# Kernel optimization log

Hardware: AMD Instinct MI355X
Metric: run time of the kernel (lower is better)

## Reference

```python
import jax, jax.numpy as jnp
from jax import lax
import numpy as np

D_MODEL = 1024
D_STATE = 16
D_CONV = 4
EXPAND = 2
D_INNER = EXPAND * D_MODEL  # 2048
BATCH = 4
SEQLEN = 2048


def setup_inputs() -> dict:
    key = jax.random.key(0)
    ks = jax.random.split(key, 8)
    s = 0.02  # small init scale for stability
    f32 = jnp.float32
    return {
        "x": jax.random.normal(ks[0], (BATCH, SEQLEN, D_MODEL), f32),
        # Linear weights stored as (in, out); torch applies x @ W.T with W (out, in) -- same math.
        "W_in": (jax.random.normal(ks[1], (D_MODEL, 2 * D_INNER), f32) * s),
        "conv_w": (jax.random.normal(ks[2], (D_INNER, 1, D_CONV), f32) * s),  # depthwise (O, I/groups=1, K)
        "conv_b": jnp.zeros((D_INNER,), f32),
        "W_xproj": (jax.random.normal(ks[3], (D_INNER, 2 * D_STATE), f32) * s),
        "W_dt": (jax.random.normal(ks[4], (D_INNER, D_INNER), f32) * s),
        "b_dt": jnp.zeros((D_INNER,), f32),
        "A_log": jnp.log(jax.random.uniform(ks[5], (D_INNER, D_STATE), f32, 1e-4, 1.0)),
        "D_param": jnp.ones((D_INNER,), f32),
        "W_out": (jax.random.normal(ks[6], (D_INNER, D_MODEL), f32) * s),
    }


def _mamba_forward(x, W_in, conv_w, conv_b, W_xproj, W_dt, b_dt, A_log, D_param, W_out):
    Bb, L, _ = x.shape
    # in_proj and split into x-branch and gate z
    xz = x @ W_in                      # (B, L, 2*d_inner)
    xc, z = jnp.split(xz, 2, axis=-1)
    # causal depthwise conv1d: torch pads both sides by d_conv-1 then slices [:L] == left-pad only
    xt = xc.transpose(0, 2, 1)         # (B, d_inner, L)
    xconv = lax.conv_general_dilated(
        xt, conv_w, window_strides=(1,), padding=[(D_CONV - 1, 0)],
        feature_group_count=D_INNER, dimension_numbers=("NCH", "OIH", "NCH"))
    xs = jax.nn.silu(xconv.transpose(0, 2, 1) + conv_b[None, None, :])  # (B, L, d_inner)
    # SSM inputs
    delta = jax.nn.softplus(xs @ W_dt + b_dt)          # (B, L, d_inner)
    Bs, Cs = jnp.split(xs @ W_xproj, 2, axis=-1)       # each (B, L, d_state)
    A = -jnp.exp(A_log)                                 # (d_inner, d_state)

    def step(h, inp):
        dt, bv, cv, xv = inp                            # (B,d_inner),(B,d_state),(B,d_state),(B,d_inner)
        dA = 1.0 + A[None] * dt[..., None]              # Euler discretization (B, d_inner, d_state)
        dB = bv[:, None, :] * (xv * dt)[..., None]
        h = h * dA + dB
        y = jnp.einsum("bds,bs->bd", h, cv) + D_param * xv
        return h, y

    inputs = (delta.transpose(1, 0, 2), Bs.transpose(1, 0, 2),
              Cs.transpose(1, 0, 2), xs.transpose(1, 0, 2))
    h0 = jnp.zeros((Bb, D_INNER, D_STATE), x.dtype)
    _, ys = lax.scan(step, h0, inputs)                  # ys: (L, B, d_inner)
    y = ys.transpose(1, 0, 2) * jax.nn.silu(z)          # gated output
    return y @ W_out                                    # (B, L, d_model)


def reference(x, W_in, conv_w, conv_b, W_xproj, W_dt, b_dt, A_log, D_param, W_out):
    return _mamba_forward(x, W_in, conv_w, conv_b, W_xproj, W_dt, b_dt, A_log, D_param, W_out)
```

## Files before the change

### kernel.cpp

```cpp
#include <hip/hip_runtime.h>

#define AS1 __attribute__((address_space(1)))
#define AS3 __attribute__((address_space(3)))

typedef unsigned short u16;
typedef unsigned int u32;
typedef __attribute__((ext_vector_type(8))) __bf16 bf16x8;
typedef __attribute__((ext_vector_type(8))) unsigned short u16x8;
typedef __attribute__((ext_vector_type(4))) float f32x4;

#define BATCH   4
#define SEQLEN  2048
#define DMODEL  1024
#define DINNER  2048
#define DSTATE  16
#define ROWS    (BATCH * SEQLEN)

__device__ __forceinline__ u16 f2bf(float f) {
  union { float f; unsigned u; } v; v.f = f;
  unsigned u = v.u;
  return (u16)((u + 0x7fffu + ((u >> 16) & 1u)) >> 16);
}
__device__ __forceinline__ float bf2f(u16 s) {
  union { unsigned u; float f; } v; v.u = ((unsigned)s) << 16;
  return v.f;
}
__device__ __forceinline__ float bflo(u32 p) { union { unsigned u; float f; } v; v.u = p << 16; return v.f; }
__device__ __forceinline__ float bfhi(u32 p) { union { unsigned u; float f; } v; v.u = p & 0xffff0000u; return v.f; }

__global__ void cast_f32_bf16(const float* __restrict__ in, u16* __restrict__ out, int n4) {
  int i = blockIdx.x * blockDim.x + threadIdx.x;
  if (i >= n4) return;
  float4 v = ((const float4*)in)[i];
  ushort4 o;
  o.x = f2bf(v.x); o.y = f2bf(v.y); o.z = f2bf(v.z); o.w = f2bf(v.w);
  ((ushort4*)out)[i] = o;
}

__global__ void transpose_cast(const float* __restrict__ in, u16* __restrict__ out, int R, int C) {
  __shared__ float tile[32][33];
  int x  = blockIdx.x * 32 + threadIdx.x;
  int y0 = blockIdx.y * 32;
#pragma unroll
  for (int j = 0; j < 32; j += 8)
    tile[threadIdx.y + j][threadIdx.x] = in[(size_t)(y0 + threadIdx.y + j) * C + x];
  __syncthreads();
  int xo  = blockIdx.y * 32 + threadIdx.x;
  int yo0 = blockIdx.x * 32;
#pragma unroll
  for (int j = 0; j < 32; j += 8)
    out[(size_t)(yo0 + threadIdx.y + j) * R + xo] = f2bf(tile[threadIdx.x][threadIdx.y + j]);
}

template<int EPI, int BN_>
__launch_bounds__(512, 1)
__global__ void gemm8p(const u16* __restrict__ A, const u16* __restrict__ Bt,
                       void* __restrict__ outp, const float* __restrict__ bias,
                       int M, int N, int K, int gn, int rr, int cc) {
  constexpr int NF   = BN_ / 64;
  constexpr int BCH  = BN_ / 64;
  constexpr int ASZ  = 256 * 64;
  constexpr int BSZ  = BN_ * 64;
  constexpr int BUFS = ASZ + BSZ;
  extern __shared__ u16 lds[];

  const int xcd = blockIdx.x & 7, kb = blockIdx.x >> 3;
  const int tpr = gn / cc;
  const int bm  = (xcd / tpr) * rr + kb / cc;
  const int bn  = (xcd % tpr) * cc + kb % cc;

  const int tid  = threadIdx.x;
  const int wave = tid >> 6, lane = tid & 63;
  const int wm = wave >> 2, wn = wave & 3;
  const int llo = lane & 15, lhi = lane >> 4;
  const size_t bm0 = (size_t)bm * 256, bn0 = (size_t)bn * BN_;
  const int NT = K >> 6;

  const u16* gA[4];
#pragma unroll
  for (int ch = 0; ch < 4; ++ch) {
    int row  = ch * 64 + (tid >> 3);
    int scol = ((tid & 7) ^ (row & 7)) << 3;
    gA[ch] = A + (bm0 + row) * (size_t)K + scol;
  }
  const u16* gB[BCH];
#pragma unroll
  for (int ch = 0; ch < BCH; ++ch) {
    int row  = ch * 64 + (tid >> 3);
    int scol = ((tid & 7) ^ (row & 7)) << 3;
    gB[ch] = Bt + (bn0 + row) * (size_t)K + scol;
  }

  const int mask = (llo & 7) << 4;
  const int ko[2] = { ((0 + lhi * 16) ^ mask) >> 1, ((64 + lhi * 16) ^ mask) >> 1 };

#define SGA(t, bsel, ch) __builtin_amdgcn_global_load_lds(                       \
    (const AS1 void*)(gA[ch] + ((size_t)(t) << 6)),                              \
    (AS3 void*)(lds + (bsel) * BUFS + (ch) * 4096 + wave * 512), 16, 0, 0)
#define SGB(t, bsel, ch) __builtin_amdgcn_global_load_lds(                       \
    (const AS1 void*)(gB[ch] + ((size_t)(t) << 6)),                              \
    (AS3 void*)(lds + (bsel) * BUFS + ASZ + (ch) * 4096 + wave * 512), 16, 0, 0)

  f32x4 acc[8][NF] = {};
  bf16x8 bfr[2][NF];

#define PHASE(la_, lb_, MH, KK, RDB, STG, WC)                                    \
  {                                                                              \
    bf16x8 af[4];                                                                \
    _Pragma("unroll") for (int m = 0; m < 4; ++m)                                \
      af[m] = *(const bf16x8*)(const void*)((la_) + (wm*128 + MH*64 + m*16 + llo)*64 + ko[KK]); \
    if (RDB) {                                                                   \
      _Pragma("unroll") for (int n = 0; n < NF; ++n)                             \
        bfr[KK][n] = *(const bf16x8*)(const void*)((lb_) + (wn*(16*NF) + n*16 + llo)*64 + ko[KK]); \
    }                                                                            \
    STG;                                                                         \
    __builtin_amdgcn_s_barrier();                                                \
    __builtin_amdgcn_s_setprio(1);                                               \
    _Pragma("unroll") for (int m = 0; m < 4; ++m)                                \
      _Pragma("unroll") for (int n = 0; n < NF; ++n)                             \
        acc[MH*4+m][n] = __builtin_amdgcn_mfma_f32_16x16x32_bf16(af[m], bfr[KK][n], acc[MH*4+m][n], 0, 0, 0); \
    __builtin_amdgcn_s_setprio(0);                                               \
    WC;                                                                          \
    __builtin_amdgcn_s_barrier();                                                \
  }

  SGA(0, 0, 0); SGA(0, 0, 2); SGB(0, 0, 0); SGB(0, 0, 1);
  if (BCH == 4) { SGB(0, 0, 2); SGB(0, 0, 3); }
  SGA(0, 0, 1); SGA(0, 0, 3);
  SGA(1, 1, 0); SGA(1, 1, 2); SGB(1, 1, 0); SGB(1, 1, 1);
  asm volatile("s_waitcnt vmcnt(4)" ::: "memory");
  __builtin_amdgcn_s_barrier();

  const u16* la0 = lds;            const u16* lb0 = lds + ASZ;
  const u16* la1 = lds + BUFS;     const u16* lb1 = la1 + ASZ;

  for (int u = 0; u < NT; u += 2) {
    const int v = u + 1;
    PHASE(la0, lb0, 0, 0, true,
          ({ if (BCH == 4) { SGB(v, 1, 2); SGB(v, 1, 3); } else { SGA(v, 1, 1); SGA(v, 1, 3); } }),
          ((void)0));
    PHASE(la0, lb0, 0, 1, true,
          ({ if (BCH == 4) { SGA(v, 1, 1); SGA(v, 1, 3); } }),
          ((void)0));
    PHASE(la0, lb0, 1, 0, false,
          ({ if (u + 2 < NT) { SGA(u + 2, 0, 0); SGA(u + 2, 0, 2); } }),
          ((void)0));
    PHASE(la0, lb0, 1, 1, false,
          ({ if (u + 2 < NT) { SGB(u + 2, 0, 0); SGB(u + 2, 0, 1); } }),
          ({ if (u + 2 < NT) asm volatile("s_waitcnt vmcnt(4)" ::: "memory");
             else            asm volatile("s_waitcnt vmcnt(0)" ::: "memory"); }));
    PHASE(la1, lb1, 0, 0, true,
          ({ if (u + 2 < NT) { if (BCH == 4) { SGB(u + 2, 0, 2); SGB(u + 2, 0, 3); }
                               else          { SGA(u + 2, 0, 1); SGA(u + 2, 0, 3); } } }),
          ((void)0));
    PHASE(la1, lb1, 0, 1, true,
          ({ if (u + 2 < NT && BCH == 4) { SGA(u + 2, 0, 1); SGA(u + 2, 0, 3); } }),
          ((void)0));
    PHASE(la1, lb1, 1, 0, false,
          ({ if (v + 2 < NT) { SGA(v + 2, 1, 0); SGA(v + 2, 1, 2); } }),
          ((void)0));
    PHASE(la1, lb1, 1, 1, false,
          ({ if (v + 2 < NT) { SGB(v + 2, 1, 0); SGB(v + 2, 1, 1); } }),
          ({ if (v + 2 < NT) asm volatile("s_waitcnt vmcnt(4)" ::: "memory");
             else            asm volatile("s_waitcnt vmcnt(0)" ::: "memory"); }));
  }
#undef PHASE
#undef SGA
#undef SGB

#pragma unroll
  for (int am = 0; am < 8; ++am) {
    const int mh = am >> 2, m = am & 3;
    const int rowb = (int)bm0 + wm * 128 + mh * 64 + m * 16 + lhi * 4;
#pragma unroll
    for (int n = 0; n < NF; ++n) {
      const int col = (int)bn0 + wn * (16 * NF) + n * 16 + llo;
#pragma unroll
      for (int r = 0; r < 4; ++r) {
        float v = acc[am][n][r];
        size_t idx = (size_t)(rowb + r) * N + col;
        if (EPI == 0) {
          ((u16*)outp)[idx] = f2bf(v);
        } else if (EPI == 1) {
          float xb = v + bias[col];
          float sp = (xb > 20.f) ? xb : log1pf(__expf(xb));
          ((u16*)outp)[idx] = f2bf(sp);
        } else {
          ((float*)outp)[idx] = v;
        }
      }
    }
  }
}

__global__ void conv_silu4(const u16* __restrict__ xz, const float* __restrict__ w,
                           const float* __restrict__ cb, u16* __restrict__ xs, int total4) {
  int idx = blockIdx.x * 256 + threadIdx.x;
  if (idx >= total4) return;
  int d4 = idx & (DINNER / 4 - 1);
  int l  = (idx >> 9) & (SEQLEN - 1);
  int b  = idx >> 20;
  int d  = d4 * 4;
  float4 wv[4];
#pragma unroll
  for (int j = 0; j < 4; ++j) wv[j] = ((const float4*)w)[d + j];
  float4 bias = *(const float4*)(cb + d);
  float acc[4] = { bias.x, bias.y, bias.z, bias.w };
#pragma unroll
  for (int k = 0; k < 4; ++k) {
    int li = l - 3 + k;
    if (li >= 0) {
      ushort4 xv = *(const ushort4*)(xz + (size_t)(b * SEQLEN + li) * (2 * DINNER) + d);
      acc[0] = fmaf((&wv[0].x)[k], bf2f(xv.x), acc[0]);
      acc[1] = fmaf((&wv[1].x)[k], bf2f(xv.y), acc[1]);
      acc[2] = fmaf((&wv[2].x)[k], bf2f(xv.z), acc[2]);
      acc[3] = fmaf((&wv[3].x)[k], bf2f(xv.w), acc[3]);
    }
  }
  ushort4 o;
  o.x = f2bf(acc[0] / (1.f + __expf(-acc[0])));
  o.y = f2bf(acc[1] / (1.f + __expf(-acc[1])));
  o.z = f2bf(acc[2] / (1.f + __expf(-acc[2])));
  o.w = f2bf(acc[3] / (1.f + __expf(-acc[3])));
  *(ushort4*)(xs + (size_t)idx * 4) = o;
}

__global__ void xproj_kernel(const u16* __restrict__ xs, const float* __restrict__ Wx,
                             float* __restrict__ outp) {
  __shared__ float part[256];
  int row = blockIdx.x;
  int tid = threadIdx.x;
  int c = tid & 31, kp = tid >> 5;
  const u16* xr = xs + (size_t)row * DINNER + kp * 256;
  const float* wp = Wx + (size_t)(kp * 256) * 32 + c;
  float acc = 0.f;
#pragma unroll 4
  for (int kk = 0; kk < 32; ++kk) {
    u16x8 xv = *(const u16x8*)(const void*)(xr + kk * 8);
#pragma unroll
    for (int j = 0; j < 8; ++j)
      acc = fmaf(bf2f(xv[j]), wp[(kk * 8 + j) * 32], acc);
  }
  part[tid] = acc;
  __syncthreads();
  if (tid < 32) {
    float s = 0.f;
#pragma unroll
    for (int p = 0; p < 8; ++p) s += part[p * 32 + tid];
    outp[(size_t)row * 32 + tid] = s;
  }
}

#define SC_NC 32
#define SC_CL 64
#define SC_LDS (2 * SC_NC * 16 * 33 * 4)

__launch_bounds__(512, 1)
__global__ void scan_v3(const u16* __restrict__ delta, const u16* __restrict__ xs,
                        const float* __restrict__ xproj, const u16* __restrict__ xz,
                        const float* __restrict__ A_log, const float* __restrict__ Dp,
                        u16* __restrict__ yg) {
  extern __shared__ float smem[];
  float* cP = smem;
  float* cH = smem + SC_NC * 16 * 33;
  const int tid = threadIdx.x;
  const int dl = tid & 15, ck = tid >> 4;
  const int b = blockIdx.x >> 6, dblk = blockIdx.x & 63;
  const int d0 = dblk * 32 + dl * 2;
  const int r0 = b * SEQLEN + ck * SC_CL;

  float A0[DSTATE], A1[DSTATE];
  {
    const f32x4* ap0 = (const f32x4*)(A_log + (size_t)d0 * DSTATE);
    const f32x4* ap1 = (const f32x4*)(A_log + (size_t)(d0 + 1) * DSTATE);
#pragma unroll
    for (int q = 0; q < 4; ++q) {
      f32x4 a0 = ap0[q], a1 = ap1[q];
#pragma unroll
      for (int j = 0; j < 4; ++j) { A0[q * 4 + j] = -__expf(a0[j]); A1[q * 4 + j] = -__expf(a1[j]); }
    }
  }

  const u32* dP = (const u32*)(delta + (size_t)r0 * DINNER + d0);
  const u32* xP = (const u32*)(xs    + (size_t)r0 * DINNER + d0);
  const u32* zP = (const u32*)(xz + (size_t)r0 * (2 * DINNER) + DINNER + d0);
  const float* bP = xproj + (size_t)r0 * 32;
  const int DW = DINNER / 2;
  const int ZW = DINNER;

  float P0[DSTATE], P1[DSTATE], H0[DSTATE], H1[DSTATE];
#pragma unroll
  for (int s = 0; s < DSTATE; ++s) { P0[s] = P1[s] = 1.f; H0[s] = H1[s] = 0.f; }
  {
    u32 dq0 = dP[0], xq0 = xP[0];
    u32 dq1 = dP[DW], xq1 = xP[DW];
    f32x4 Bn[4];
#pragma unroll
    for (int q = 0; q < 4; ++q) Bn[q] = ((const f32x4*)bP)[q];
    for (int l = 0; l < SC_CL; ++l) {
      const u32 dc = dq0, xc = xq0;
      dq0 = dq1; xq0 = xq1;
      if (l + 2 < SC_CL) { dq1 = dP[(l + 2) * DW]; xq1 = xP[(l + 2) * DW]; }
      f32x4 Bc[4] = { Bn[0], Bn[1], Bn[2], Bn[3] };
      if (l + 1 < SC_CL) {
        const f32x4* bn = (const f32x4*)(bP + (l + 1) * 32);
#pragma unroll
        for (int q = 0; q < 4; ++q) Bn[q] = bn[q];
      }
      float dt0 = bflo(dc), dt1 = bfhi(dc);
      float x0 = bflo(xc),  x1 = bfhi(xc);
      float dtx0 = dt0 * x0, dtx1 = dt1 * x1;
#pragma unroll
      for (int s = 0; s < DSTATE; ++s) {
        float bs = Bc[s >> 2][s & 3];
        float dA0 = fmaf(A0[s], dt0, 1.f);
        float dA1 = fmaf(A1[s], dt1, 1.f);
        P0[s] *= dA0; P1[s] *= dA1;
        H0[s] = fmaf(H0[s], dA0, bs * dtx0);
        H1[s] = fmaf(H1[s], dA1, bs * dtx1);
      }
    }
  }
  {
    float* p = cP + (ck * 16 + dl) * 33;
    float* h = cH + (ck * 16 + dl) * 33;
#pragma unroll
    for (int s = 0; s < DSTATE; ++s) {
      p[s] = P0[s]; p[16 + s] = P1[s];
      h[s] = H0[s]; h[16 + s] = H1[s];
    }
  }
  __syncthreads();

  {
    const int s2 = tid & 15, dd = tid >> 4;
    const int idx = (dd & 1) * 16 + s2;
    float* pbase = cP + (dd >> 1) * 33 + idx;
    float* hbase = cH + (dd >> 1) * 33 + idx;
    float h = 0.f;
    for (int c = 0; c < SC_NC; ++c) {
      float p = pbase[c * 16 * 33], hh = hbase[c * 16 * 33];
      pbase[c * 16 * 33] = h;
      h = fmaf(p, h, hh);
    }
  }
  __syncthreads();

  float h0[DSTATE], h1[DSTATE];
  {
    const float* p = cP + (ck * 16 + dl) * 33;
#pragma unroll
    for (int s = 0; s < DSTATE; ++s) { h0[s] = p[s]; h1[s] = p[16 + s]; }
  }
  const float Dv0 = Dp[d0], Dv1 = Dp[d0 + 1];
  u32* yP = (u32*)(yg + (size_t)r0 * DINNER + d0);
  {
    u32 dq0 = dP[0], xq0 = xP[0], zq0 = zP[0];
    u32 dq1 = dP[DW], xq1 = xP[DW], zq1 = zP[ZW];
    f32x4 Bn[4], Cn[4];
#pragma unroll
    for (int q = 0; q < 4; ++q) { Bn[q] = ((const f32x4*)bP)[q]; Cn[q] = ((const f32x4*)bP)[q + 4]; }
    for (int l = 0; l < SC_CL; ++l) {
      const u32 dc = dq0, xc = xq0, zc = zq0;
      dq0 = dq1; xq0 = xq1; zq0 = zq1;
      if (l + 2 < SC_CL) { dq1 = dP[(l + 2) * DW]; xq1 = xP[(l + 2) * DW]; zq1 = zP[(l + 2) * ZW]; }
      f32x4 Bc[4] = { Bn[0], Bn[1], Bn[2], Bn[3] };
      f32x4 Cc[4] = { Cn[0], Cn[1], Cn[2], Cn[3] };
      if (l + 1 < SC_CL) {
        const f32x4* bn = (const f32x4*)(bP + (l + 1) * 32);
#pragma unroll
        for (int q = 0; q < 4; ++q) { Bn[q] = bn[q]; Cn[q] = bn[q + 4]; }
      }
      float dt0 = bflo(dc), dt1 = bfhi(dc);
      float x0 = bflo(xc),  x1 = bfhi(xc);
      float dtx0 = dt0 * x0, dtx1 = dt1 * x1;
      float yp0 = 0.f, yp1 = 0.f;
#pragma unroll
      for (int s = 0; s < DSTATE; ++s) {
        float bs = Bc[s >> 2][s & 3];
        float cs = Cc[s >> 2][s & 3];
        float dA0 = fmaf(A0[s], dt0, 1.f);
        float dA1 = fmaf(A1[s], dt1, 1.f);
        h0[s] = fmaf(h0[s], dA0, bs * dtx0);
        h1[s] = fmaf(h1[s], dA1, bs * dtx1);
        yp0 = fmaf(h0[s], cs, yp0);
        yp1 = fmaf(h1[s], cs, yp1);
      }
      float z0 = bflo(zc), z1 = bfhi(zc);
      float y0 = (yp0 + Dv0 * x0) * (z0 / (1.f + __expf(-z0)));
      float y1 = (yp1 + Dv1 * x1) * (z1 / (1.f + __expf(-z1)));
      yP[l * DW] = (u32)f2bf(y0) | ((u32)f2bf(y1) << 16);
    }
  }
}

extern "C" void kernel_launch(void* const* d_in, const int* in_sizes, int n_in,
                              void* d_out, int out_size, void* d_ws, size_t ws_size,
                              hipStream_t stream) {
  const float* x       = (const float*)d_in[0];
  const float* W_in    = (const float*)d_in[1];
  const float* conv_w  = (const float*)d_in[2];
  const float* conv_b  = (const float*)d_in[3];
  const float* W_xproj = (const float*)d_in[4];
  const float* W_dt    = (const float*)d_in[5];
  const float* b_dt    = (const float*)d_in[6];
  const float* A_log   = (const float*)d_in[7];
  const float* D_param = (const float*)d_in[8];
  const float* W_out   = (const float*)d_in[9];
  float* out = (float*)d_out;

  char* ws = (char*)d_ws;
  const size_t MB = 1ull << 20;
  u16*   x_bf  = (u16*)(ws);
  u16*   WinT  = (u16*)(ws + 16 * MB);
  u16*   WdtT  = (u16*)(ws + 24 * MB);
  u16*   xz_bf = (u16*)(ws + 32 * MB);
  u16*   xs_bf = (u16*)(ws + 96 * MB);
  u16*   delta = (u16*)(ws + 128 * MB);
  float* xpj   = (float*)(ws + 192 * MB);
  u16*   WoutT = (u16*)(ws + 193 * MB);
  u16*   yg    = (u16*)(ws);

  hipFuncSetAttribute((const void*)gemm8p<0, 256>, hipFuncAttributeMaxDynamicSharedMemorySize, 131072);
  hipFuncSetAttribute((const void*)gemm8p<1, 256>, hipFuncAttributeMaxDynamicSharedMemorySize, 131072);
  hipFuncSetAttribute((const void*)gemm8p<2, 128>, hipFuncAttributeMaxDynamicSharedMemorySize, 98304);
  hipFuncSetAttribute((const void*)scan_v3, hipFuncAttributeMaxDynamicSharedMemorySize, SC_LDS);

  dim3 tb(32, 8);

  cast_f32_bf16<<<(ROWS * DMODEL / 4 + 255) / 256, 256, 0, stream>>>(x, x_bf, ROWS * DMODEL / 4);
  transpose_cast<<<dim3((2 * DINNER) / 32, DMODEL / 32), tb, 0, stream>>>(W_in, WinT, DMODEL, 2 * DINNER);
  transpose_cast<<<dim3(DINNER / 32, DINNER / 32), tb, 0, stream>>>(W_dt, WdtT, DINNER, DINNER);
  transpose_cast<<<dim3(DMODEL / 32, DINNER / 32), tb, 0, stream>>>(W_out, WoutT, DINNER, DMODEL);

  gemm8p<0, 256><<<512, 512, 131072, stream>>>(x_bf, WinT, xz_bf, nullptr,
                                               ROWS, 2 * DINNER, DMODEL, 16, 8, 8);

  conv_silu4<<<(ROWS * DINNER / 4) / 256, 256, 0, stream>>>(
      xz_bf, conv_w, conv_b, xs_bf, ROWS * DINNER / 4);

  gemm8p<1, 256><<<256, 512, 131072, stream>>>(xs_bf, WdtT, delta, b_dt,
                                               ROWS, DINNER, DINNER, 8, 4, 8);

  xproj_kernel<<<ROWS, 256, 0, stream>>>(xs_bf, W_xproj, xpj);

  scan_v3<<<BATCH * (DINNER / 32), 512, SC_LDS, stream>>>(
      delta, xs_bf, xpj, xz_bf, A_log, D_param, yg);

  gemm8p<2, 128><<<256, 512, 98304, stream>>>(yg, WoutT, out, nullptr,
                                              ROWS, DMODEL, DINNER, 8, 4, 8);
}
```

Measured before the change: 476.5 us.

## Replace 256-wide 8-wave GEMM with 128x128 4-wave multi-block GEMM

Swaps the hand-scheduled 256xN tile GEMM (512 threads, one block per CU, large dynamic LDS, 8-phase interleaved pipeline) for a simpler 128x128 tile kernel with K-step 32, static LDS double buffering and up to three blocks per CU. The goal is to use more concurrent blocks to hide latency and cut the tail on the three projection GEMMs, in place of intra-block software pipelining. The cost is lower data reuse per tile, more global traffic, a full block sync every K step, and no LDS swizzle, so bank conflicts may appear.

```diff
diff --git a/kernel.cpp b/kernel.cpp
--- a/kernel.cpp
+++ b/kernel.cpp
@@ -27,6 +27,16 @@
 }
 __device__ __forceinline__ float bflo(u32 p) { union { unsigned u; float f; } v; v.u = p << 16; return v.f; }
 __device__ __forceinline__ float bfhi(u32 p) { union { unsigned u; float f; } v; v.u = p & 0xffff0000u; return v.f; }
+
+template<int IMM>
+__device__ __forceinline__ bf16x8 dsr(unsigned addr) {
+  bf16x8 r;
+  asm volatile("ds_read_b128 %0, %1 offset:%2" : "=&v"(r) : "v"(addr), "i"(IMM));
+  return r;
+}
+__device__ __forceinline__ unsigned lds_addr(const u16* p) {
+  return (unsigned)(size_t)(const AS3 u16*)p;
+}
 
 __global__ void cast_f32_bf16(const float* __restrict__ in, u16* __restrict__ out, int n4) {
   int i = blockIdx.x * blockDim.x + threadIdx.x;
@@ -52,132 +62,90 @@
     out[(size_t)(yo0 + threadIdx.y + j) * R + xo] = f2bf(tile[threadIdx.x][threadIdx.y + j]);
 }
 
-template<int EPI, int BN_>
-__launch_bounds__(512, 1)
-__global__ void gemm8p(const u16* __restrict__ A, const u16* __restrict__ Bt,
-                       void* __restrict__ outp, const float* __restrict__ bias,
-                       int M, int N, int K, int gn, int rr, int cc) {
-  constexpr int NF   = BN_ / 64;
-  constexpr int BCH  = BN_ / 64;
-  constexpr int ASZ  = 256 * 64;
-  constexpr int BSZ  = BN_ * 64;
-  constexpr int BUFS = ASZ + BSZ;
-  extern __shared__ u16 lds[];
+template<int EPI>
+__launch_bounds__(256, 3)
+__global__ void gemm128(const u16* __restrict__ A, const u16* __restrict__ Bt,
+                        void* __restrict__ outp, const float* __restrict__ bias,
+                        int M, int N, int K, int gnt, int rr, int cc) {
+  __shared__ u16 lds[2][2][128 * 32];
 
   const int xcd = blockIdx.x & 7, kb = blockIdx.x >> 3;
-  const int tpr = gn / cc;
-  const int bm  = (xcd / tpr) * rr + kb / cc;
-  const int bn  = (xcd % tpr) * cc + kb % cc;
+  const int xcols = gnt / cc;
+  const int bm = (xcd / xcols) * rr + kb / cc;
+  const int bn = (xcd % xcols) * cc + kb % cc;
 
   const int tid  = threadIdx.x;
   const int wave = tid >> 6, lane = tid & 63;
-  const int wm = wave >> 2, wn = wave & 3;
+  const int wm = wave >> 1, wn = wave & 1;
   const int llo = lane & 15, lhi = lane >> 4;
-  const size_t bm0 = (size_t)bm * 256, bn0 = (size_t)bn * BN_;
-  const int NT = K >> 6;
-
-  const u16* gA[4];
-#pragma unroll
-  for (int ch = 0; ch < 4; ++ch) {
-    int row  = ch * 64 + (tid >> 3);
-    int scol = ((tid & 7) ^ (row & 7)) << 3;
-    gA[ch] = A + (bm0 + row) * (size_t)K + scol;
-  }
-  const u16* gB[BCH];
-#pragma unroll
-  for (int ch = 0; ch < BCH; ++ch) {
-    int row  = ch * 64 + (tid >> 3);
-    int scol = ((tid & 7) ^ (row & 7)) << 3;
-    gB[ch] = Bt + (bn0 + row) * (size_t)K + scol;
-  }
-
-  const int mask = (llo & 7) << 4;
-  const int ko[2] = { ((0 + lhi * 16) ^ mask) >> 1, ((64 + lhi * 16) ^ mask) >> 1 };
-
-#define SGA(t, bsel, ch) __builtin_amdgcn_global_load_lds(                       \
-    (const AS1 void*)(gA[ch] + ((size_t)(t) << 6)),                              \
-    (AS3 void*)(lds + (bsel) * BUFS + (ch) * 4096 + wave * 512), 16, 0, 0)
-#define SGB(t, bsel, ch) __builtin_amdgcn_global_load_lds(                       \
-    (const AS1 void*)(gB[ch] + ((size_t)(t) << 6)),                              \
-    (AS3 void*)(lds + (bsel) * BUFS + ASZ + (ch) * 4096 + wave * 512), 16, 0, 0)
-
-  f32x4 acc[8][NF] = {};
-  bf16x8 bfr[2][NF];
-
-#define PHASE(la_, lb_, MH, KK, RDB, STG, WC)                                    \
-  {                                                                              \
-    bf16x8 af[4];                                                                \
-    _Pragma("unroll") for (int m = 0; m < 4; ++m)                                \
-      af[m] = *(const bf16x8*)(const void*)((la_) + (wm*128 + MH*64 + m*16 + llo)*64 + ko[KK]); \
-    if (RDB) {                                                                   \
-      _Pragma("unroll") for (int n = 0; n < NF; ++n)                             \
-        bfr[KK][n] = *(const bf16x8*)(const void*)((lb_) + (wn*(16*NF) + n*16 + llo)*64 + ko[KK]); \
-    }                                                                            \
-    STG;                                                                         \
-    __builtin_amdgcn_s_barrier();                                                \
-    __builtin_amdgcn_s_setprio(1);                                               \
-    _Pragma("unroll") for (int m = 0; m < 4; ++m)                                \
-      _Pragma("unroll") for (int n = 0; n < NF; ++n)                             \
-        acc[MH*4+m][n] = __builtin_amdgcn_mfma_f32_16x16x32_bf16(af[m], bfr[KK][n], acc[MH*4+m][n], 0, 0, 0); \
-    __builtin_amdgcn_s_setprio(0);                                               \
-    WC;                                                                          \
-    __builtin_amdgcn_s_barrier();                                                \
-  }
-
-  SGA(0, 0, 0); SGA(0, 0, 2); SGB(0, 0, 0); SGB(0, 0, 1);
-  if (BCH == 4) { SGB(0, 0, 2); SGB(0, 0, 3); }
-  SGA(0, 0, 1); SGA(0, 0, 3);
-  SGA(1, 1, 0); SGA(1, 1, 2); SGB(1, 1, 0); SGB(1, 1, 1);
-  asm volatile("s_waitcnt vmcnt(4)" ::: "memory");
-  __builtin_amdgcn_s_barrier();
-
-  const u16* la0 = lds;            const u16* lb0 = lds + ASZ;
-  const u16* la1 = lds + BUFS;     const u16* lb1 = la1 + ASZ;
-
-  for (int u = 0; u < NT; u += 2) {
-    const int v = u + 1;
-    PHASE(la0, lb0, 0, 0, true,
-          ({ if (BCH == 4) { SGB(v, 1, 2); SGB(v, 1, 3); } else { SGA(v, 1, 1); SGA(v, 1, 3); } }),
-          ((void)0));
-    PHASE(la0, lb0, 0, 1, true,
-          ({ if (BCH == 4) { SGA(v, 1, 1); SGA(v, 1, 3); } }),
-          ((void)0));
-    PHASE(la0, lb0, 1, 0, false,
-          ({ if (u + 2 < NT) { SGA(u + 2, 0, 0); SGA(u + 2, 0, 2); } }),
-          ((void)0));
-    PHASE(la0, lb0, 1, 1, false,
-          ({ if (u + 2 < NT) { SGB(u + 2, 0, 0); SGB(u + 2, 0, 1); } }),
-          ({ if (u + 2 < NT) asm volatile("s_waitcnt vmcnt(4)" ::: "memory");
-             else            asm volatile("s_waitcnt vmcnt(0)" ::: "memory"); }));
-    PHASE(la1, lb1, 0, 0, true,
-          ({ if (u + 2 < NT) { if (BCH == 4) { SGB(u + 2, 0, 2); SGB(u + 2, 0, 3); }
-                               else          { SGA(u + 2, 0, 1); SGA(u + 2, 0, 3); } } }),
-          ((void)0));
-    PHASE(la1, lb1, 0, 1, true,
-          ({ if (u + 2 < NT && BCH == 4) { SGA(u + 2, 0, 1); SGA(u + 2, 0, 3); } }),
-          ((void)0));
-    PHASE(la1, lb1, 1, 0, false,
-          ({ if (v + 2 < NT) { SGA(v + 2, 1, 0); SGA(v + 2, 1, 2); } }),
-          ((void)0));
-    PHASE(la1, lb1, 1, 1, false,
-          ({ if (v + 2 < NT) { SGB(v + 2, 1, 0); SGB(v + 2, 1, 1); } }),
-          ({ if (v + 2 < NT) asm volatile("s_waitcnt vmcnt(4)" ::: "memory");
-             else            asm volatile("s_waitcnt vmcnt(0)" ::: "memory"); }));
-  }
-#undef PHASE
-#undef SGA
-#undef SGB
-
-#pragma unroll
-  for (int am = 0; am < 8; ++am) {
-    const int mh = am >> 2, m = am & 3;
-    const int rowb = (int)bm0 + wm * 128 + mh * 64 + m * 16 + lhi * 4;
-#pragma unroll
-    for (int n = 0; n < NF; ++n) {
-      const int col = (int)bn0 + wn * (16 * NF) + n * 16 + llo;
+  const size_t bm0 = (size_t)bm * 128, bn0 = (size_t)bn * 128;
+  const int NT = K >> 5;
+
+  const u16* gA[2]; const u16* gB[2];
+#pragma unroll
+  for (int c = 0; c < 2; ++c) {
+    int idx = c * 256 + tid;
+    int row = idx >> 2, slot = idx & 3;
+    gA[c] = A  + (bm0 + row) * (size_t)K + slot * 8;
+    gB[c] = Bt + (bn0 + row) * (size_t)K + slot * 8;
+  }
+
+  unsigned aA[2], aB[2];
+  {
+    const unsigned base = lds_addr(&lds[0][0][0]);
+#pragma unroll
+    for (int b = 0; b < 2; ++b) {
+      aA[b] = base + b * 16384u + (unsigned)(wm * 64 + llo) * 64u + lhi * 16u;
+      aB[b] = base + b * 16384u + 8192u + (unsigned)(wn * 64 + llo) * 64u + lhi * 16u;
+    }
+  }
+
+#define STG(t, b) do {                                                            \
+    _Pragma("unroll")                                                             \
+    for (int c = 0; c < 2; ++c) {                                                 \
+      __builtin_amdgcn_global_load_lds((const AS1 void*)(gA[c] + ((size_t)(t) << 5)), \
+          (AS3 void*)(&lds[b][0][(c * 256 + tid) * 8]), 16, 0, 0);                \
+      __builtin_amdgcn_global_load_lds((const AS1 void*)(gB[c] + ((size_t)(t) << 5)), \
+          (AS3 void*)(&lds[b][1][(c * 256 + tid) * 8]), 16, 0, 0);                \
+    }                                                                             \
+  } while (0)
+
+  f32x4 acc[4][4] = {};
+
+  STG(0, 0);
+  __syncthreads();
+
+  for (int t = 0; t < NT; ++t) {
+    const int cur = t & 1;
+    if (t + 1 < NT) STG(t + 1, cur ^ 1);
+    bf16x8 af[4], bf[4];
+    {
+      const unsigned a = aA[cur], b = aB[cur];
+      af[0] = dsr<0>(a);    af[1] = dsr<1024>(a);
+      af[2] = dsr<2048>(a); af[3] = dsr<3072>(a);
+      bf[0] = dsr<0>(b);    bf[1] = dsr<1024>(b);
+      bf[2] = dsr<2048>(b); bf[3] = dsr<3072>(b);
+    }
+    asm volatile("s_waitcnt lgkmcnt(0)" ::: "memory");
+    __builtin_amdgcn_sched_barrier(0);
+#pragma unroll
+    for (int m = 0; m < 4; ++m)
+#pragma unroll
+      for (int n = 0; n < 4; ++n)
+        acc[m][n] = __builtin_amdgcn_mfma_f32_16x16x32_bf16(af[m], bf[n], acc[m][n], 0, 0, 0);
+    __syncthreads();
+  }
+#undef STG
+
+#pragma unroll
+  for (int m = 0; m < 4; ++m) {
+    const int rowb = (int)bm0 + wm * 64 + m * 16 + lhi * 4;
+#pragma unroll
+    for (int n = 0; n < 4; ++n) {
+      const int col = (int)bn0 + wn * 64 + n * 16 + llo;
 #pragma unroll
       for (int r = 0; r < 4; ++r) {
-        float v = acc[am][n][r];
+        float v = acc[m][n][r];
         size_t idx = (size_t)(rowb + r) * N + col;
         if (EPI == 0) {
           ((u16*)outp)[idx] = f2bf(v);
@@ -421,9 +389,6 @@
   u16*   WoutT = (u16*)(ws + 193 * MB);
   u16*   yg    = (u16*)(ws);
 
-  hipFuncSetAttribute((const void*)gemm8p<0, 256>, hipFuncAttributeMaxDynamicSharedMemorySize, 131072);
-  hipFuncSetAttribute((const void*)gemm8p<1, 256>, hipFuncAttributeMaxDynamicSharedMemorySize, 131072);
-  hipFuncSetAttribute((const void*)gemm8p<2, 128>, hipFuncAttributeMaxDynamicSharedMemorySize, 98304);
   hipFuncSetAttribute((const void*)scan_v3, hipFuncAttributeMaxDynamicSharedMemorySize, SC_LDS);
 
   dim3 tb(32, 8);
@@ -433,20 +398,20 @@
   transpose_cast<<<dim3(DINNER / 32, DINNER / 32), tb, 0, stream>>>(W_dt, WdtT, DINNER, DINNER);
   transpose_cast<<<dim3(DMODEL / 32, DINNER / 32), tb, 0, stream>>>(W_out, WoutT, DINNER, DMODEL);
 
-  gemm8p<0, 256><<<512, 512, 131072, stream>>>(x_bf, WinT, xz_bf, nullptr,
-                                               ROWS, 2 * DINNER, DMODEL, 16, 8, 8);
+  gemm128<0><<<2048, 256, 0, stream>>>(x_bf, WinT, xz_bf, nullptr,
+                                       ROWS, 2 * DINNER, DMODEL, 32, 32, 8);
 
   conv_silu4<<<(ROWS * DINNER / 4) / 256, 256, 0, stream>>>(
       xz_bf, conv_w, conv_b, xs_bf, ROWS * DINNER / 4);
 
-  gemm8p<1, 256><<<256, 512, 131072, stream>>>(xs_bf, WdtT, delta, b_dt,
-                                               ROWS, DINNER, DINNER, 8, 4, 8);
+  gemm128<1><<<1024, 256, 0, stream>>>(xs_bf, WdtT, delta, b_dt,
+                                       ROWS, DINNER, DINNER, 16, 32, 4);
 
   xproj_kernel<<<ROWS, 256, 0, stream>>>(xs_bf, W_xproj, xpj);
 
   scan_v3<<<BATCH * (DINNER / 32), 512, SC_LDS, stream>>>(
       delta, xs_bf, xpj, xz_bf, A_log, D_param, yg);
 
-  gemm8p<2, 128><<<256, 512, 98304, stream>>>(yg, WoutT, out, nullptr,
-                                              ROWS, DMODEL, DINNER, 8, 4, 8);
-}
+  gemm128<2><<<512, 256, 0, stream>>>(yg, WoutT, out, nullptr,
+                                      ROWS, DMODEL, DINNER, 8, 16, 4);
+}
```

Result: slower. 497.2 us (+4.3%).
